# Performance work log

Measured on AMD Instinct MI355X. Metric: run time of the kernel, lower is better.

Reference implementation:

```python
import jax, jax.numpy as jnp
from jax import lax
import numpy as np

PROPAGATE = 3  # propagate_size; avg_pool2d(3,1,pad=1)*9 == 3x3 zero-padded sum pool
EPS = 1e-07


def setup_inputs() -> dict:
    key = jax.random.key(0)
    k1, k2 = jax.random.split(key)
    foreground = jax.random.normal(k1, (4, 64, 64, 64), dtype=jnp.float32)
    masks = jax.random.uniform(k2, (4, 1, 64, 64), dtype=jnp.float32)
    return {"foreground": foreground, "masks": masks}


def _sum_pool3x3(x):
    # x: [b, p, h, w]; 3x3 stride-1 zero-padded sum (== avg_pool2d(3,1,pad=1) * 9)
    return lax.reduce_window(x, 0.0, lax.add,
                             window_dimensions=(1, 1, PROPAGATE, PROPAGATE),
                             window_strides=(1, 1, 1, 1),
                             padding=[(0, 0), (0, 0), (1, 1), (1, 1)])


def reference(foreground, masks):
    # First-call forward of KnowledgeConsistentAttention (att_scores_prev is None;
    # masks/ratio are only stored as state and do not affect this output).
    bz, nc, h, w = foreground.shape
    # dynamic 1x1 kernels: one kernel per spatial location -> [b, h*w, nc]
    kern = foreground.reshape(bz, nc, h * w).transpose(0, 2, 1) + EPS
    kern = kern / jnp.sqrt(jnp.sum(kern ** 2, axis=-1, keepdims=True))
    # conv2d with per-image 1x1 kernels == per-pixel dot products
    scores = jnp.einsum('bpc,bcyx->bpyx', kern, foreground)  # [b, h*w, h, w]
    scores = _sum_pool3x3(scores)
    att = jax.nn.softmax(scores, axis=1)
    # conv_transpose2d with the same 1x1 kernels == weighted sum of kernels
    out = jnp.einsum('bpc,bpyx->bcyx', kern, att)  # [b, nc, h, w]
    return out
```

## Files before the change

### kernel.cpp

```cpp
#include <hip/hip_runtime.h>


typedef __bf16 bf16_t;
typedef __bf16 bf16x2 __attribute__((ext_vector_type(2)));
typedef __bf16 bf16x8 __attribute__((ext_vector_type(8)));
typedef float f32x4 __attribute__((ext_vector_type(4)));

#define HW_ 4096
#define CH 64

static __device__ __forceinline__ void gload_lds16(const void* gsrc, void* lds_dst) {
  __builtin_amdgcn_global_load_lds(
      (const __attribute__((address_space(1))) unsigned int*)gsrc,
      (__attribute__((address_space(3))) unsigned int*)lds_dst, 16, 0, 0);
}

static __device__ __forceinline__ int pack_bf16x2(float a, float b) {
  bf16x2 p; p[0] = (bf16_t)a; p[1] = (bf16_t)b;
  return __builtin_bit_cast(int, p);
}

__global__ __launch_bounds__(1024, 1) void kca_prep(const float* __restrict__ fg,
                                                    char* __restrict__ KpB,
                                                    char* __restrict__ KBB,
                                                    char* __restrict__ GtB) {
  const int b = blockIdx.x >> 6, y = blockIdx.x & 63;
  const int t = threadIdx.x;
  const float* F = fg + (size_t)b * (CH * HW_);

  __shared__ float  Ft[3 * 64 * 64];
  __shared__ bf16_t Ks[64 * 72];
  __shared__ bf16_t Gs[64 * 72];
  __shared__ float  red[16][64];
  __shared__ float  rn[64];

#pragma unroll
  for (int k = 0; k < 3; ++k) {
    const int o = t + k * 1024;
    const int r = o >> 10, c = (o >> 4) & 63, x4 = o & 15;
    const int gy = y - 1 + r;
    f32x4 v = {0.f, 0.f, 0.f, 0.f};
    if (gy >= 0 && gy <= 63) v = *(const f32x4*)(F + c * HW_ + gy * 64 + x4 * 4);
    *(f32x4*)&Ft[o * 4] = v;
  }
  __syncthreads();

  const int x = t & 63, c0 = t >> 6;
  float v4[4], g4[4], ssq = 0.f;
#pragma unroll
  for (int i = 0; i < 4; ++i) {
    const int c = c0 * 4 + i;
    const float v = Ft[4096 + c * 64 + x] + 1e-7f;
    v4[i] = v; ssq = fmaf(v, v, ssq);
    float s = 0.f;
#pragma unroll
    for (int r = 0; r < 3; ++r) {
      const float* row = &Ft[r * 4096 + c * 64];
      float vv = row[x];
      if (x > 0)  vv += row[x - 1];
      if (x < 63) vv += row[x + 1];
      s += vv;
    }
    g4[i] = s * 1.4426950408889634f;
  }
  red[c0][x] = ssq;
  __syncthreads();
  if (t < 512) red[t >> 6][t & 63] += red[(t >> 6) + 8][t & 63];
  __syncthreads();
  if (t < 256) red[t >> 6][t & 63] += red[(t >> 6) + 4][t & 63];
  __syncthreads();
  if (t < 64) rn[t] = 1.0f / sqrtf(red[0][t] + red[1][t] + red[2][t] + red[3][t]);
  __syncthreads();
  {
    const float rv = rn[x];
    bf16x2* ksp = (bf16x2*)((char*)Ks + x * 144 + c0 * 8);
    bf16x2* gsp = (bf16x2*)((char*)Gs + x * 144 + c0 * 8);
    bf16x2 k0; k0[0] = (bf16_t)(v4[0] * rv); k0[1] = (bf16_t)(v4[1] * rv);
    bf16x2 k1; k1[0] = (bf16_t)(v4[2] * rv); k1[1] = (bf16_t)(v4[3] * rv);
    bf16x2 g0; g0[0] = (bf16_t)g4[0]; g0[1] = (bf16_t)g4[1];
    bf16x2 g1; g1[0] = (bf16_t)g4[2]; g1[1] = (bf16_t)g4[3];
    ksp[0] = k0; ksp[1] = k1;
    gsp[0] = g0; gsp[1] = g1;
  }
  __syncthreads();

  char* Kp_b = KpB + (size_t)b * (HW_ * CH * 2) + (size_t)y * 8192;
  char* Gt_b = GtB + (size_t)b * (HW_ * CH * 2) + (size_t)y * 8192;
  char* KB_b = KBB + (size_t)b * (HW_ * CH * 2);
  if (t < 512) {
    const int row = t >> 3, colb = (t & 7) * 16;
    *(bf16x8*)(Kp_b + row * 128 + colb) = *(const bf16x8*)((char*)Ks + row * 144 + colb);
    const int tile = t >> 8;
    const int mt   = (t >> 6) & 3;
    const int ln   = t & 63;
    const int l15_ = ln & 15, lg_ = ln >> 4;
    bf16x8 kv;
#pragma unroll
    for (int j = 0; j < 8; ++j) {
      const int pl = tile * 32 + 16 * (j >> 2) + 4 * lg_ + (j & 3);
      kv[j] = Ks[pl * 72 + 16 * mt + l15_];
    }
    *(bf16x8*)(KB_b + (size_t)(2 * y + tile) * 4096 + mt * 1024 + ln * 16) = kv;
  } else {
    const int s = t - 512;
    const int row = s >> 3, colb = (s & 7) * 16;
    *(bf16x8*)(Gt_b + row * 128 + colb) = *(const bf16x8*)((char*)Gs + row * 144 + colb);
  }
}

__global__ __launch_bounds__(1024, 4) void kca_attn(const char* __restrict__ KpB,
                                                    const char* __restrict__ KBB,
                                                    const char* __restrict__ GtB,
                                                    float* __restrict__ out) {
  const int sw_id = ((blockIdx.x & 7) << 5) | (blockIdx.x >> 3);
  const int b = sw_id >> 6, y = sw_id & 63;
  const int t = threadIdx.x;
  const int lane = t & 63, w = t >> 6;
  const int g = w & 7;
  const int st = w >> 3;
  const int l15 = lane & 15, lg = lane >> 4;

  const char* Kp_b = KpB + (size_t)b * (HW_ * CH * 2);
  const char* KB_b = KBB + (size_t)b * (HW_ * CH * 2);
  const char* Gt_b = GtB + (size_t)b * (HW_ * CH * 2);
  float* Ob = out + (size_t)b * (CH * HW_);

  __shared__ __align__(16) char SM[69632];
  __shared__ float mll[8][64];
  __shared__ float linv[64];

  char* KpG = SM + g * 8192;

  bf16x8 qb00, qb01, qb10, qb11;
  {
    const char* qr0 = Gt_b + (size_t)(y * 64 + st * 32 + l15) * 128;
    const char* qr1 = qr0 + 16 * 128;
    qb00 = *(const bf16x8*)(qr0 + 16 * lg);
    qb01 = *(const bf16x8*)(qr0 + 64 + 16 * lg);
    qb10 = *(const bf16x8*)(qr1 + 16 * lg);
    qb11 = *(const bf16x8*)(qr1 + 64 + 16 * lg);
  }

  const int cA = st * 128 + lane, cB = cA + 64;
  const int rA1 = cA >> 3, rB1 = cB >> 3;
  const size_t kpoffA = (size_t)rA1 * 128 + (((cA & 7) * 16) ^ ((rA1 & 7) << 4));
  const size_t kpoffB = (size_t)rB1 * 128 + (((cB & 7) * 16) ^ ((rB1 & 7) << 4));

#define STAGE_KP(D, P0)                                                          \
  do {                                                                           \
    gload_lds16(Kp_b + (size_t)(P0) * 128 + kpoffA, KpG + (D) * 4096 + cA * 16); \
    gload_lds16(Kp_b + (size_t)(P0) * 128 + kpoffB, KpG + (D) * 4096 + cB * 16); \
  } while (0)

  f32x4 oaccT[2][4];
#pragma unroll
  for (int s = 0; s < 2; ++s)
#pragma unroll
    for (int mt = 0; mt < 4; ++mt) { oaccT[s][mt][0]=0.f; oaccT[s][mt][1]=0.f; oaccT[s][mt][2]=0.f; oaccT[s][mt][3]=0.f; }
  float lpart0 = 0.f, lpart1 = 0.f;

  const int pb0 = g * 512;
  STAGE_KP(0, pb0);
  int cur = 0;
  for (int it = 0; it < 16; ++it) {
    __syncthreads();
    const char* kbp = KB_b + (size_t)(g * 16 + it) * 4096 + lane * 16;
    const bf16x8 kb0 = *(const bf16x8*)(kbp);
    const bf16x8 kb1 = *(const bf16x8*)(kbp + 1024);
    const bf16x8 kb2 = *(const bf16x8*)(kbp + 2048);
    const bf16x8 kb3 = *(const bf16x8*)(kbp + 3072);
    if (it + 1 < 16) STAGE_KP(cur ^ 1, pb0 + (it + 1) * 32);

    const char* kp = KpG + cur * 4096;
    f32x4 S[2][2];
#pragma unroll
    for (int f = 0; f < 2; ++f) {
      const int r = f * 16 + l15, swr = (r & 7) << 4;
      bf16x8 a0 = *(const bf16x8*)(kp + r * 128 + ((16 * lg) ^ swr));
      bf16x8 a1 = *(const bf16x8*)(kp + r * 128 + ((64 + 16 * lg) ^ swr));
      f32x4 z0 = {0.f, 0.f, 0.f, 0.f};
      z0 = __builtin_amdgcn_mfma_f32_16x16x32_bf16(a0, qb00, z0, 0, 0, 0);
      z0 = __builtin_amdgcn_mfma_f32_16x16x32_bf16(a1, qb01, z0, 0, 0, 0);
      S[0][f] = z0;
      f32x4 z1 = {0.f, 0.f, 0.f, 0.f};
      z1 = __builtin_amdgcn_mfma_f32_16x16x32_bf16(a0, qb10, z1, 0, 0, 0);
      z1 = __builtin_amdgcn_mfma_f32_16x16x32_bf16(a1, qb11, z1, 0, 0, 0);
      S[1][f] = z1;
    }

    union { int wd[4]; bf16x8 v; } pa0, pa1;
    {
      const float e0 = exp2f(S[0][0][0]), e1 = exp2f(S[0][0][1]);
      const float e2 = exp2f(S[0][0][2]), e3 = exp2f(S[0][0][3]);
      const float e4 = exp2f(S[0][1][0]), e5 = exp2f(S[0][1][1]);
      const float e6 = exp2f(S[0][1][2]), e7 = exp2f(S[0][1][3]);
      lpart0 += ((e0 + e1) + (e2 + e3)) + ((e4 + e5) + (e6 + e7));
      pa0.wd[0] = pack_bf16x2(e0, e1); pa0.wd[1] = pack_bf16x2(e2, e3);
      pa0.wd[2] = pack_bf16x2(e4, e5); pa0.wd[3] = pack_bf16x2(e6, e7);
    }
    {
      const float e0 = exp2f(S[1][0][0]), e1 = exp2f(S[1][0][1]);
      const float e2 = exp2f(S[1][0][2]), e3 = exp2f(S[1][0][3]);
      const float e4 = exp2f(S[1][1][0]), e5 = exp2f(S[1][1][1]);
      const float e6 = exp2f(S[1][1][2]), e7 = exp2f(S[1][1][3]);
      lpart1 += ((e0 + e1) + (e2 + e3)) + ((e4 + e5) + (e6 + e7));
      pa1.wd[0] = pack_bf16x2(e0, e1); pa1.wd[1] = pack_bf16x2(e2, e3);
      pa1.wd[2] = pack_bf16x2(e4, e5); pa1.wd[3] = pack_bf16x2(e6, e7);
    }

    oaccT[0][0] = __builtin_amdgcn_mfma_f32_16x16x32_bf16(pa0.v, kb0, oaccT[0][0], 0, 0, 0);
    oaccT[1][0] = __builtin_amdgcn_mfma_f32_16x16x32_bf16(pa1.v, kb0, oaccT[1][0], 0, 0, 0);
    oaccT[0][1] = __builtin_amdgcn_mfma_f32_16x16x32_bf16(pa0.v, kb1, oaccT[0][1], 0, 0, 0);
    oaccT[1][1] = __builtin_amdgcn_mfma_f32_16x16x32_bf16(pa1.v, kb1, oaccT[1][1], 0, 0, 0);
    oaccT[0][2] = __builtin_amdgcn_mfma_f32_16x16x32_bf16(pa0.v, kb2, oaccT[0][2], 0, 0, 0);
    oaccT[1][2] = __builtin_amdgcn_mfma_f32_16x16x32_bf16(pa1.v, kb2, oaccT[1][2], 0, 0, 0);
    oaccT[0][3] = __builtin_amdgcn_mfma_f32_16x16x32_bf16(pa0.v, kb3, oaccT[0][3], 0, 0, 0);
    oaccT[1][3] = __builtin_amdgcn_mfma_f32_16x16x32_bf16(pa1.v, kb3, oaccT[1][3], 0, 0, 0);
    cur ^= 1;
  }
#undef STAGE_KP

  lpart0 += __shfl_xor(lpart0, 16); lpart0 += __shfl_xor(lpart0, 32);
  lpart1 += __shfl_xor(lpart1, 16); lpart1 += __shfl_xor(lpart1, 32);
  if (lg == 0) {
    mll[g][st * 32 + l15]      = lpart0;
    mll[g][st * 32 + 16 + l15] = lpart1;
  }
  __syncthreads();
  if (t < 64) {
    float L = 0.f;
#pragma unroll
    for (int k = 0; k < 8; ++k) L += mll[k][t];
    linv[t] = 1.0f / L;
  }
  float* Rg = (float*)SM + (g >> 1) * 4352;
  if ((g & 1) == 0) {
#pragma unroll
    for (int s = 0; s < 2; ++s)
#pragma unroll
      for (int mt = 0; mt < 4; ++mt)
#pragma unroll
        for (int r = 0; r < 4; ++r)
          Rg[(16 * mt + l15) * 68 + st * 32 + s * 16 + 4 * lg + r] = oaccT[s][mt][r];
  }
  __syncthreads();
  if (g & 1) {
#pragma unroll
    for (int s = 0; s < 2; ++s)
#pragma unroll
      for (int mt = 0; mt < 4; ++mt)
#pragma unroll
        for (int r = 0; r < 4; ++r)
          Rg[(16 * mt + l15) * 68 + st * 32 + s * 16 + 4 * lg + r] += oaccT[s][mt][r];
  }
  __syncthreads();
  {
    const int c = t >> 4, q4 = (t & 15) * 4;
    const float* R0 = (const float*)SM;
    f32x4 v = *(const f32x4*)(R0 + c * 68 + q4);
    v += *(const f32x4*)(R0 + 4352 + c * 68 + q4);
    v += *(const f32x4*)(R0 + 8704 + c * 68 + q4);
    v += *(const f32x4*)(R0 + 13056 + c * 68 + q4);
    const f32x4 li = *(const f32x4*)(linv + q4);
    f32x4 o;
#pragma unroll
    for (int j = 0; j < 4; ++j) o[j] = v[j] * li[j];
    *(f32x4*)(Ob + (size_t)c * HW_ + y * 64 + q4) = o;
  }
}

extern "C" void kernel_launch(void* const* d_in, const int* in_sizes, int n_in,
                              void* d_out, int out_size, void* d_ws, size_t ws_size,
                              hipStream_t stream) {
  const float* fg = (const float*)d_in[0];
  float* out = (float*)d_out;
  char* ws = (char*)d_ws;
  char* Kp = ws;
  char* KB = ws + (2u << 20);
  char* Gt = ws + (4u << 20);
  hipLaunchKernelGGL(kca_prep, dim3(256), dim3(1024), 0, stream, fg, Kp, KB, Gt);
  hipLaunchKernelGGL(kca_attn, dim3(256), dim3(1024), 0, stream, Kp, KB, Gt, out);
}
```

Before: 44.03 us.

## Load score-GEMM operands straight to registers with double buffering, dropping LDS staging

The per-iteration staging of the Kp tile through LDS via global_load_lds, and the block-wide __syncthreads it needed, are removed. Each wave now loads its own A fragments directly from global memory into registers, software-pipelined with two register sets across an unrolled-by-two loop. MFMA sections are also bracketed with s_setprio to favour matrix issue. The aim is to eliminate barrier stalls across the 16 waves. In exchange, the two waves sharing a tile now load it redundantly from cache, which raises register pressure. The final prefetch also reads past the wave's range, possibly past the end of the buffer for the last batch.

```diff
diff --git a/kernel.cpp b/kernel.cpp
--- a/kernel.cpp
+++ b/kernel.cpp
@@ -8,12 +8,6 @@
 
 #define HW_ 4096
 #define CH 64
-
-static __device__ __forceinline__ void gload_lds16(const void* gsrc, void* lds_dst) {
-  __builtin_amdgcn_global_load_lds(
-      (const __attribute__((address_space(1))) unsigned int*)gsrc,
-      (__attribute__((address_space(3))) unsigned int*)lds_dst, 16, 0, 0);
-}
 
 static __device__ __forceinline__ int pack_bf16x2(float a, float b) {
   bf16x2 p; p[0] = (bf16_t)a; p[1] = (bf16_t)b;
@@ -129,8 +123,6 @@
   __shared__ float mll[8][64];
   __shared__ float linv[64];
 
-  char* KpG = SM + g * 8192;
-
   bf16x8 qb00, qb01, qb10, qb11;
   {
     const char* qr0 = Gt_b + (size_t)(y * 64 + st * 32 + l15) * 128;
@@ -141,17 +133,6 @@
     qb11 = *(const bf16x8*)(qr1 + 64 + 16 * lg);
   }
 
-  const int cA = st * 128 + lane, cB = cA + 64;
-  const int rA1 = cA >> 3, rB1 = cB >> 3;
-  const size_t kpoffA = (size_t)rA1 * 128 + (((cA & 7) * 16) ^ ((rA1 & 7) << 4));
-  const size_t kpoffB = (size_t)rB1 * 128 + (((cB & 7) * 16) ^ ((rB1 & 7) << 4));
-
-#define STAGE_KP(D, P0)                                                          \
-  do {                                                                           \
-    gload_lds16(Kp_b + (size_t)(P0) * 128 + kpoffA, KpG + (D) * 4096 + cA * 16); \
-    gload_lds16(Kp_b + (size_t)(P0) * 128 + kpoffB, KpG + (D) * 4096 + cB * 16); \
-  } while (0)
-
   f32x4 oaccT[2][4];
 #pragma unroll
   for (int s = 0; s < 2; ++s)
@@ -160,65 +141,77 @@
   float lpart0 = 0.f, lpart1 = 0.f;
 
   const int pb0 = g * 512;
-  STAGE_KP(0, pb0);
-  int cur = 0;
-  for (int it = 0; it < 16; ++it) {
-    __syncthreads();
-    const char* kbp = KB_b + (size_t)(g * 16 + it) * 4096 + lane * 16;
-    const bf16x8 kb0 = *(const bf16x8*)(kbp);
-    const bf16x8 kb1 = *(const bf16x8*)(kbp + 1024);
-    const bf16x8 kb2 = *(const bf16x8*)(kbp + 2048);
-    const bf16x8 kb3 = *(const bf16x8*)(kbp + 3072);
-    if (it + 1 < 16) STAGE_KP(cur ^ 1, pb0 + (it + 1) * 32);
-
-    const char* kp = KpG + cur * 4096;
-    f32x4 S[2][2];
-#pragma unroll
-    for (int f = 0; f < 2; ++f) {
-      const int r = f * 16 + l15, swr = (r & 7) << 4;
-      bf16x8 a0 = *(const bf16x8*)(kp + r * 128 + ((16 * lg) ^ swr));
-      bf16x8 a1 = *(const bf16x8*)(kp + r * 128 + ((64 + 16 * lg) ^ swr));
-      f32x4 z0 = {0.f, 0.f, 0.f, 0.f};
-      z0 = __builtin_amdgcn_mfma_f32_16x16x32_bf16(a0, qb00, z0, 0, 0, 0);
-      z0 = __builtin_amdgcn_mfma_f32_16x16x32_bf16(a1, qb01, z0, 0, 0, 0);
-      S[0][f] = z0;
-      f32x4 z1 = {0.f, 0.f, 0.f, 0.f};
-      z1 = __builtin_amdgcn_mfma_f32_16x16x32_bf16(a0, qb10, z1, 0, 0, 0);
-      z1 = __builtin_amdgcn_mfma_f32_16x16x32_bf16(a1, qb11, z1, 0, 0, 0);
-      S[1][f] = z1;
-    }
-
-    union { int wd[4]; bf16x8 v; } pa0, pa1;
-    {
-      const float e0 = exp2f(S[0][0][0]), e1 = exp2f(S[0][0][1]);
-      const float e2 = exp2f(S[0][0][2]), e3 = exp2f(S[0][0][3]);
-      const float e4 = exp2f(S[0][1][0]), e5 = exp2f(S[0][1][1]);
-      const float e6 = exp2f(S[0][1][2]), e7 = exp2f(S[0][1][3]);
-      lpart0 += ((e0 + e1) + (e2 + e3)) + ((e4 + e5) + (e6 + e7));
-      pa0.wd[0] = pack_bf16x2(e0, e1); pa0.wd[1] = pack_bf16x2(e2, e3);
-      pa0.wd[2] = pack_bf16x2(e4, e5); pa0.wd[3] = pack_bf16x2(e6, e7);
-    }
-    {
-      const float e0 = exp2f(S[1][0][0]), e1 = exp2f(S[1][0][1]);
-      const float e2 = exp2f(S[1][0][2]), e3 = exp2f(S[1][0][3]);
-      const float e4 = exp2f(S[1][1][0]), e5 = exp2f(S[1][1][1]);
-      const float e6 = exp2f(S[1][1][2]), e7 = exp2f(S[1][1][3]);
-      lpart1 += ((e0 + e1) + (e2 + e3)) + ((e4 + e5) + (e6 + e7));
-      pa1.wd[0] = pack_bf16x2(e0, e1); pa1.wd[1] = pack_bf16x2(e2, e3);
-      pa1.wd[2] = pack_bf16x2(e4, e5); pa1.wd[3] = pack_bf16x2(e6, e7);
-    }
-
-    oaccT[0][0] = __builtin_amdgcn_mfma_f32_16x16x32_bf16(pa0.v, kb0, oaccT[0][0], 0, 0, 0);
-    oaccT[1][0] = __builtin_amdgcn_mfma_f32_16x16x32_bf16(pa1.v, kb0, oaccT[1][0], 0, 0, 0);
-    oaccT[0][1] = __builtin_amdgcn_mfma_f32_16x16x32_bf16(pa0.v, kb1, oaccT[0][1], 0, 0, 0);
-    oaccT[1][1] = __builtin_amdgcn_mfma_f32_16x16x32_bf16(pa1.v, kb1, oaccT[1][1], 0, 0, 0);
-    oaccT[0][2] = __builtin_amdgcn_mfma_f32_16x16x32_bf16(pa0.v, kb2, oaccT[0][2], 0, 0, 0);
-    oaccT[1][2] = __builtin_amdgcn_mfma_f32_16x16x32_bf16(pa1.v, kb2, oaccT[1][2], 0, 0, 0);
-    oaccT[0][3] = __builtin_amdgcn_mfma_f32_16x16x32_bf16(pa0.v, kb3, oaccT[0][3], 0, 0, 0);
-    oaccT[1][3] = __builtin_amdgcn_mfma_f32_16x16x32_bf16(pa1.v, kb3, oaccT[1][3], 0, 0, 0);
-    cur ^= 1;
-  }
-#undef STAGE_KP
+  const char* arf0 = Kp_b + (size_t)(pb0 + l15) * 128 + 16 * lg;
+  const char* arf1 = arf0 + 16 * 128;
+  const char* kbp0 = KB_b + (size_t)(g * 16) * 4096 + lane * 16;
+
+  bf16x8 Aa0, Aa1, Aa2, Aa3, Ba0, Ba1, Ba2, Ba3;
+  Aa0 = *(const bf16x8*)(arf0);        Aa1 = *(const bf16x8*)(arf0 + 64);
+  Aa2 = *(const bf16x8*)(arf1);        Aa3 = *(const bf16x8*)(arf1 + 64);
+
+#define COMPUTE(A0, A1, A2, A3, KBP)                                             \
+  do {                                                                           \
+    const bf16x8 kb0 = *(const bf16x8*)(KBP);                                    \
+    const bf16x8 kb1 = *(const bf16x8*)((KBP) + 1024);                           \
+    const bf16x8 kb2 = *(const bf16x8*)((KBP) + 2048);                           \
+    const bf16x8 kb3 = *(const bf16x8*)((KBP) + 3072);                           \
+    f32x4 z00 = {0.f,0.f,0.f,0.f}, z01 = {0.f,0.f,0.f,0.f};                      \
+    f32x4 z10 = {0.f,0.f,0.f,0.f}, z11 = {0.f,0.f,0.f,0.f};                      \
+    __builtin_amdgcn_s_setprio(1);                                               \
+    z00 = __builtin_amdgcn_mfma_f32_16x16x32_bf16(A0, qb00, z00, 0, 0, 0);       \
+    z00 = __builtin_amdgcn_mfma_f32_16x16x32_bf16(A1, qb01, z00, 0, 0, 0);       \
+    z01 = __builtin_amdgcn_mfma_f32_16x16x32_bf16(A2, qb00, z01, 0, 0, 0);       \
+    z01 = __builtin_amdgcn_mfma_f32_16x16x32_bf16(A3, qb01, z01, 0, 0, 0);       \
+    z10 = __builtin_amdgcn_mfma_f32_16x16x32_bf16(A0, qb10, z10, 0, 0, 0);       \
+    z10 = __builtin_amdgcn_mfma_f32_16x16x32_bf16(A1, qb11, z10, 0, 0, 0);       \
+    z11 = __builtin_amdgcn_mfma_f32_16x16x32_bf16(A2, qb10, z11, 0, 0, 0);       \
+    z11 = __builtin_amdgcn_mfma_f32_16x16x32_bf16(A3, qb11, z11, 0, 0, 0);       \
+    __builtin_amdgcn_s_setprio(0);                                               \
+    union { int wd[4]; bf16x8 v; } pa0, pa1;                                     \
+    {                                                                            \
+      const float e0 = exp2f(z00[0]), e1 = exp2f(z00[1]);                        \
+      const float e2 = exp2f(z00[2]), e3 = exp2f(z00[3]);                        \
+      const float e4 = exp2f(z01[0]), e5 = exp2f(z01[1]);                        \
+      const float e6 = exp2f(z01[2]), e7 = exp2f(z01[3]);                        \
+      lpart0 += ((e0 + e1) + (e2 + e3)) + ((e4 + e5) + (e6 + e7));               \
+      pa0.wd[0] = pack_bf16x2(e0, e1); pa0.wd[1] = pack_bf16x2(e2, e3);          \
+      pa0.wd[2] = pack_bf16x2(e4, e5); pa0.wd[3] = pack_bf16x2(e6, e7);          \
+    }                                                                            \
+    {                                                                            \
+      const float e0 = exp2f(z10[0]), e1 = exp2f(z10[1]);                        \
+      const float e2 = exp2f(z10[2]), e3 = exp2f(z10[3]);                        \
+      const float e4 = exp2f(z11[0]), e5 = exp2f(z11[1]);                        \
+      const float e6 = exp2f(z11[2]), e7 = exp2f(z11[3]);                        \
+      lpart1 += ((e0 + e1) + (e2 + e3)) + ((e4 + e5) + (e6 + e7));               \
+      pa1.wd[0] = pack_bf16x2(e0, e1); pa1.wd[1] = pack_bf16x2(e2, e3);          \
+      pa1.wd[2] = pack_bf16x2(e4, e5); pa1.wd[3] = pack_bf16x2(e6, e7);          \
+    }                                                                            \
+    __builtin_amdgcn_s_setprio(1);                                               \
+    oaccT[0][0] = __builtin_amdgcn_mfma_f32_16x16x32_bf16(pa0.v, kb0, oaccT[0][0], 0, 0, 0); \
+    oaccT[1][0] = __builtin_amdgcn_mfma_f32_16x16x32_bf16(pa1.v, kb0, oaccT[1][0], 0, 0, 0); \
+    oaccT[0][1] = __builtin_amdgcn_mfma_f32_16x16x32_bf16(pa0.v, kb1, oaccT[0][1], 0, 0, 0); \
+    oaccT[1][1] = __builtin_amdgcn_mfma_f32_16x16x32_bf16(pa1.v, kb1, oaccT[1][1], 0, 0, 0); \
+    oaccT[0][2] = __builtin_amdgcn_mfma_f32_16x16x32_bf16(pa0.v, kb2, oaccT[0][2], 0, 0, 0); \
+    oaccT[1][2] = __builtin_amdgcn_mfma_f32_16x16x32_bf16(pa1.v, kb2, oaccT[1][2], 0, 0, 0); \
+    oaccT[0][3] = __builtin_amdgcn_mfma_f32_16x16x32_bf16(pa0.v, kb3, oaccT[0][3], 0, 0, 0); \
+    oaccT[1][3] = __builtin_amdgcn_mfma_f32_16x16x32_bf16(pa1.v, kb3, oaccT[1][3], 0, 0, 0); \
+    __builtin_amdgcn_s_setprio(0);                                               \
+  } while (0)
+
+  for (int it = 0; it < 16; it += 2) {
+    const char* ar0 = arf0 + (size_t)(it + 1) * 4096;
+    const char* ar1 = arf1 + (size_t)(it + 1) * 4096;
+    Ba0 = *(const bf16x8*)(ar0);       Ba1 = *(const bf16x8*)(ar0 + 64);
+    Ba2 = *(const bf16x8*)(ar1);       Ba3 = *(const bf16x8*)(ar1 + 64);
+    COMPUTE(Aa0, Aa1, Aa2, Aa3, kbp0 + (size_t)it * 4096);
+
+    const char* ar2 = arf0 + (size_t)(it + 2) * 4096;
+    const char* ar3 = arf1 + (size_t)(it + 2) * 4096;
+    Aa0 = *(const bf16x8*)(ar2);       Aa1 = *(const bf16x8*)(ar2 + 64);
+    Aa2 = *(const bf16x8*)(ar3);       Aa3 = *(const bf16x8*)(ar3 + 64);
+    COMPUTE(Ba0, Ba1, Ba2, Ba3, kbp0 + (size_t)(it + 1) * 4096);
+  }
+#undef COMPUTE
 
   lpart0 += __shfl_xor(lpart0, 16); lpart0 += __shfl_xor(lpart0, 32);
   lpart1 += __shfl_xor(lpart1, 16); lpart1 += __shfl_xor(lpart1, 32);
```

New measurement: 78.75 us. 1.79x slower.
